# Kernel tuning notes

Measured on AMD Instinct MI355X. Metric: run time of the kernel, lower is better.

The kernel has to match this reference:

```python
import jax, jax.numpy as jnp
import numpy as np
from jax import lax

B, T, H, L, NV = 2048, 100, 256, 128, 5  # batch, max_len, hidden, latent, len(NUC_VOCAB)


def setup_inputs() -> dict:
    key = jax.random.key(0)
    ks = jax.random.split(key, 13)
    s = 0.05
    inp = {
        "x_seq": jax.random.uniform(ks[0], (B, T, NV), dtype=jnp.float32),
        "hidden_states": jax.random.normal(ks[1], (B, H), dtype=jnp.float32) * 0.1,
        "tree_latent_vec": jax.random.normal(ks[2], (B, L), dtype=jnp.float32),
        "graph_latent_vec": jax.random.normal(ks[3], (B, L), dtype=jnp.float32),
        "lengths": jnp.maximum(1, jax.random.randint(ks[4], (B,), 0, T + 1)).astype(jnp.int32),
        # concat_squash_linear: (H + L) -> H
        "W_cs": jax.random.normal(ks[5], (H + L, H), dtype=jnp.float32) * s,
        "b_cs": jnp.zeros((H,), dtype=jnp.float32),
        # GRU cell linears: (H + NV) -> H, acting on cat([x, h])
        "W_z": jax.random.normal(ks[6], (NV + H, H), dtype=jnp.float32) * s,
        "b_z": jnp.zeros((H,), dtype=jnp.float32),
        "W_r": jax.random.normal(ks[7], (NV + H, H), dtype=jnp.float32) * s,
        "b_r": jnp.zeros((H,), dtype=jnp.float32),
        "W_h": jax.random.normal(ks[8], (NV + H, H), dtype=jnp.float32) * s,
        "b_h": jnp.zeros((H,), dtype=jnp.float32),
    }
    return inp


def _decode(x_seq, hidden_states, tree_latent_vec, graph_latent_vec, lengths,
            W_cs, b_cs, W_z, b_z, W_r, b_r, W_h, b_h):
    # concat volatile hidden state with graph latent, squash back to H
    h0 = jax.nn.relu(jnp.concatenate([hidden_states, graph_latent_vec], axis=-1) @ W_cs + b_cs)

    def gru_step(h, x):  # h: [B,H], x: [B,NV]
        xh = jnp.concatenate([x, h], axis=-1)          # [B, NV+H]
        z = jax.nn.sigmoid(xh @ W_z + b_z)
        r = jax.nn.sigmoid(xh @ W_r + b_r)
        xg = jnp.concatenate([x, r * h], axis=-1)
        pre_h = jnp.tanh(xg @ W_h + b_h)
        new_h = (1.0 - z) * h + z * pre_h
        return new_h, new_h

    _, hs = lax.scan(gru_step, h0, jnp.swapaxes(x_seq, 0, 1))  # [T,B,H]
    all_h = jnp.swapaxes(hs, 0, 1)                              # [B,T,H]

    # gather hidden state at last valid timestep (pre_padding_idx)
    new_h = jnp.take_along_axis(all_h, (lengths - 1)[:, None, None], axis=1)[:, 0]  # [B,H]

    # per-segment max-pool over valid positions (segment_representation)
    mask = jnp.arange(T)[None, :] < lengths[:, None]            # [B,T]
    seg_rep = jnp.max(jnp.where(mask[:, :, None], all_h, -jnp.inf), axis=1)  # [B,H]

    # depadded token features concatenated with per-batch tree/graph latents;
    # kept padded [B,T,.] with zeros at invalid positions (fixed-shape form)
    tok = jnp.concatenate([
        all_h,
        jnp.broadcast_to(tree_latent_vec[:, None, :], (B, T, L)),
        jnp.broadcast_to(graph_latent_vec[:, None, :], (B, T, L)),
    ], axis=-1)                                                 # [B,T,H+2L]
    all_hidden_states = jnp.where(mask[:, :, None], tok, 0.0)
    return new_h, all_hidden_states, seg_rep


def reference(x_seq, hidden_states, tree_latent_vec, graph_latent_vec, lengths,
              W_cs, b_cs, W_z, b_z, W_r, b_r, W_h, b_h):
    return _decode(x_seq, hidden_states, tree_latent_vec, graph_latent_vec, lengths,
                   W_cs, b_cs, W_z, b_z, W_r, b_r, W_h, b_h)
```

## Files before the change

kernel.cpp:

```cpp
#include <hip/hip_runtime.h>
#include <stdint.h>

#define B_N 2048
#define T_N 100
#define H_N 256
#define L_N 128
#define NV_N 5
#define COLS (H_N + 2 * 128)

#define KXH 261
#define KPAD 264
#define KCS 384
#define RB 8
#define NKQ 8
#define KQ_LEN 33
#define CH 11

static constexpr long long OUT_ALLH = (long long)B_N * H_N;
static constexpr long long OUT_SEG  = OUT_ALLH + (long long)B_N * T_N * COLS;

static constexpr int SMEM_FLOATS = 2 * NKQ * RB * H_N + 2 * KPAD * RB;
static constexpr int SMEM_BYTES  = SMEM_FLOATS * 4;

__device__ __forceinline__ float bits2f(uint32_t u) {
    union { uint32_t u; float f; } v; v.u = u; return v.f;
}
__device__ __forceinline__ uint16_t f2bf(float f) {
    union { float f; uint32_t u; } v; v.f = f;
    uint32_t r = (v.u + 0x7FFFu + ((v.u >> 16) & 1u)) >> 16;
    return (uint16_t)r;
}

__device__ __forceinline__ int detect_f32(const uint32_t* __restrict__ w) {
    int cnt = 0;
    #pragma unroll 8
    for (int i = 0; i < 64; ++i) {
        uint32_t e = (w[i] >> 23) & 0xFFu;
        cnt += (e >= 97u && e <= 130u) ? 1 : 0;
    }
    return cnt >= 32 ? 1 : 0;
}

template <bool F32> struct IO;

template <> struct IO<true> {
    using Raw = float4;
    static __device__ __forceinline__ Raw ldraw(const void* p, long long idx) {
        return *(const float4*)((const float*)p + idx);
    }
    static __device__ __forceinline__ void cvt(const Raw& u, float f[4]) {
        f[0] = u.x; f[1] = u.y; f[2] = u.z; f[3] = u.w;
    }
    static __device__ __forceinline__ void ld4(const void* p, long long idx, float f[4]) {
        const float4 v = *(const float4*)((const float*)p + idx);
        f[0] = v.x; f[1] = v.y; f[2] = v.z; f[3] = v.w;
    }
    static __device__ __forceinline__ float ld1(const void* p, long long idx) {
        return ((const float*)p)[idx];
    }
    static __device__ __forceinline__ void st4(void* p, long long idx, const float f[4]) {
        *(float4*)((float*)p + idx) = make_float4(f[0], f[1], f[2], f[3]);
    }
    static __device__ __forceinline__ void st4z(void* p, long long idx) {
        *(float4*)((float*)p + idx) = make_float4(0.f, 0.f, 0.f, 0.f);
    }
};

template <> struct IO<false> {
    using Raw = uint2;
    static __device__ __forceinline__ Raw ldraw(const void* p, long long idx) {
        return *(const uint2*)((const uint16_t*)p + idx);
    }
    static __device__ __forceinline__ void cvt(const Raw& u, float f[4]) {
        f[0] = bits2f(u.x << 16);
        f[1] = bits2f(u.x & 0xFFFF0000u);
        f[2] = bits2f(u.y << 16);
        f[3] = bits2f(u.y & 0xFFFF0000u);
    }
    static __device__ __forceinline__ void ld4(const void* p, long long idx, float f[4]) {
        uint2 u = *(const uint2*)((const uint16_t*)p + idx);
        cvt(u, f);
    }
    static __device__ __forceinline__ float ld1(const void* p, long long idx) {
        return bits2f(((uint32_t)((const uint16_t*)p)[idx]) << 16);
    }
    static __device__ __forceinline__ void st4(void* p, long long idx, const float f[4]) {
        uint2 u;
        u.x = (uint32_t)f2bf(f[0]) | ((uint32_t)f2bf(f[1]) << 16);
        u.y = (uint32_t)f2bf(f[2]) | ((uint32_t)f2bf(f[3]) << 16);
        *(uint2*)((uint16_t*)p + idx) = u;
    }
    static __device__ __forceinline__ void st4z(void* p, long long idx) {
        *(uint2*)((uint16_t*)p + idx) = make_uint2(0u, 0u);
    }
};

__device__ __forceinline__ float sigmoid_f(float x) {
    x = fminf(fmaxf(x, -30.f), 30.f);
    return 1.f / (1.f + __expf(-x));
}
__device__ __forceinline__ float tanh_f(float x) {
    x = fminf(fmaxf(x, -15.f), 15.f);
    float e = __expf(-2.f * x);
    return (1.f - e) / (1.f + e);
}

template <bool F32>
__global__ __launch_bounds__(256) void latent_fill_kernel(
    const void* __restrict__ tree,
    const void* __restrict__ graph,
    const int* __restrict__ lengths,
    const void* __restrict__ Wcs_detect,
    void* __restrict__ out)
{
    __shared__ int s_is32;
    if (threadIdx.x == 0) s_is32 = detect_f32((const uint32_t*)Wcs_detect);
    __syncthreads();
    if ((s_is32 != 0) != F32) return;

    long long idx = (long long)blockIdx.x * 256 + threadIdx.x;
    int c = ((int)(idx & 31)) * 8;
    long long bt = idx >> 5;
    int t = (int)(bt % T_N);
    int b = (int)(bt / T_N);

    long long dst = OUT_ALLH + bt * COLS + H_N + c;
    if (t < lengths[b]) {
        float v[8];
        if (c < L_N) {
            IO<F32>::ld4(tree, (long long)b * L_N + c, v);
            IO<F32>::ld4(tree, (long long)b * L_N + c + 4, v + 4);
        } else {
            IO<F32>::ld4(graph, (long long)b * L_N + (c - L_N), v);
            IO<F32>::ld4(graph, (long long)b * L_N + (c - L_N) + 4, v + 4);
        }
        IO<F32>::st4(out, dst, v);
        IO<F32>::st4(out, dst + 4, v + 4);
    } else {
        IO<F32>::st4z(out, dst);
        IO<F32>::st4z(out, dst + 4);
    }
}

template <bool F32>
__global__ __launch_bounds__(512, 2) void gru_kernel(
    const void* __restrict__ x_seq,
    const void* __restrict__ hidden,
    const void* __restrict__ graph,
    const int* __restrict__ lengths,
    const void* __restrict__ Wcs, const void* __restrict__ bcs,
    const void* __restrict__ Wz,  const void* __restrict__ bz,
    const void* __restrict__ Wr,  const void* __restrict__ br,
    const void* __restrict__ Wh,  const void* __restrict__ bh,
    void* __restrict__ out)
{
    extern __shared__ float smem[];
    float* Pz  = smem;
    float* Pr  = Pz  + NKQ * RB * H_N;
    float* xhT = Pr  + NKQ * RB * H_N;
    float* xgT = xhT + KPAD * RB;

    __shared__ int s_is32;
    __shared__ int s_len[RB];
    if (threadIdx.x == 0) s_is32 = detect_f32((const uint32_t*)Wcs);
    __syncthreads();
    if ((s_is32 != 0) != F32) return;

    const int tid  = threadIdx.x;
    const int wv   = tid >> 6;
    const int lane = tid & 63;
    const int c0   = lane * 4;

    if (tid < RB) {
        int L = lengths[blockIdx.x * RB + tid];
        s_len[tid] = min(max(L, 1), T_N);
    }
    if (tid < (KPAD - KXH) * RB) {
        int p = tid / RB, r = tid - p * RB;
        xhT[(KXH + p) * RB + r] = 0.f;
        xgT[(KXH + p) * RB + r] = 0.f;
    }
    __syncthreads();

    const int b0  = blockIdx.x * RB;
    const int bo  = b0 + wv;
    const int len = s_len[wv];
    int maxlen = 1;
    #pragma unroll
    for (int i = 0; i < RB; ++i) maxlen = max(maxlen, s_len[i]);

    {
        float* cs = Pz;
        for (int i = tid; i < RB * KCS; i += 512) {
            int r = i / KCS;
            int k = i - r * KCS;
            int bb = b0 + r;
            float v = (k < H_N) ? IO<F32>::ld1(hidden, (long long)bb * H_N + k)
                                : IO<F32>::ld1(graph,  (long long)bb * L_N + (k - H_N));
            cs[r * 388 + k] = v;
        }
    }
    __syncthreads();

    float h[4];
    {
        const float* cs = Pz;
        float acc[4];
        IO<F32>::ld4(bcs, c0, acc);
        for (int k = 0; k < KCS; k += 4) {
            const float4 hv = *reinterpret_cast<const float4*>(&cs[wv * 388 + k]);
            float hvv[4] = {hv.x, hv.y, hv.z, hv.w};
            #pragma unroll
            for (int kk = 0; kk < 4; ++kk) {
                float w[4];
                IO<F32>::ld4(Wcs, (long long)(k + kk) * H_N + c0, w);
                #pragma unroll
                for (int j = 0; j < 4; ++j) acc[j] += hvv[kk] * w[j];
            }
        }
        #pragma unroll
        for (int j = 0; j < 4; ++j) h[j] = fmaxf(acc[j], 0.f);
    }
    __syncthreads();

    float bzv[4], brv[4], bhv[4];
    IO<F32>::ld4(bz, c0, bzv);
    IO<F32>::ld4(br, c0, brv);
    IO<F32>::ld4(bh, c0, bhv);

    float smax[4] = {-1e30f, -1e30f, -1e30f, -1e30f};

    const int xr = tid / NV_N;
    const int xi = tid - xr * NV_N;
    float xv = 0.f;
    if (tid < RB * NV_N)
        xv = IO<F32>::ld1(x_seq, ((long long)(b0 + xr) * T_N + 0) * NV_N + xi);

    if (tid < RB * NV_N) {
        xhT[xi * RB + xr] = xv;
        xgT[xi * RB + xr] = xv;
    }
    #pragma unroll
    for (int j = 0; j < 4; ++j)
        xhT[(NV_N + c0 + j) * RB + wv] = h[j];
    if (tid < RB * NV_N) {
        int tn = (1 < T_N) ? 1 : 0;
        xv = IO<F32>::ld1(x_seq, ((long long)(b0 + xr) * T_N + tn) * NV_N + xi);
    }
    __syncthreads();

    const int k0 = wv * KQ_LEN;

    float z[4];

    for (int t = 0; t < maxlen; ++t) {
        float az[8][4], ar[8][4];
        #pragma unroll
        for (int r = 0; r < 8; ++r)
            #pragma unroll
            for (int j = 0; j < 4; ++j) { az[r][j] = 0.f; ar[r][j] = 0.f; }

        #pragma unroll 1
        for (int ch = 0; ch < 3; ++ch) {
            const int kb = k0 + ch * CH;
            typename IO<F32>::Raw rz[CH], rr[CH];
            #pragma unroll
            for (int i = 0; i < CH; ++i) {
                const int k  = kb + i;
                const int kl = (k <= KXH - 1) ? k : (KXH - 1);
                rz[i] = IO<F32>::ldraw(Wz, (long long)kl * H_N + c0);
                rr[i] = IO<F32>::ldraw(Wr, (long long)kl * H_N + c0);
            }
            #pragma unroll
            for (int i = 0; i < CH; ++i) {
                const int k = kb + i;
                const float4 a = *reinterpret_cast<const float4*>(&xhT[k * RB + 0]);
                const float4 b = *reinterpret_cast<const float4*>(&xhT[k * RB + 4]);
                float hv[8] = {a.x, a.y, a.z, a.w, b.x, b.y, b.z, b.w};
                float wz4[4], wr4[4];
                IO<F32>::cvt(rz[i], wz4);
                IO<F32>::cvt(rr[i], wr4);
                #pragma unroll
                for (int r = 0; r < 8; ++r) {
                    #pragma unroll
                    for (int j = 0; j < 4; ++j) {
                        az[r][j] += hv[r] * wz4[j];
                        ar[r][j] += hv[r] * wr4[j];
                    }
                }
            }
        }
        #pragma unroll
        for (int r = 0; r < 8; ++r) {
            *reinterpret_cast<float4*>(&Pz[(wv * RB + r) * H_N + c0]) =
                make_float4(az[r][0], az[r][1], az[r][2], az[r][3]);
            *reinterpret_cast<float4*>(&Pr[(wv * RB + r) * H_N + c0]) =
                make_float4(ar[r][0], ar[r][1], ar[r][2], ar[r][3]);
        }
        __syncthreads();

        {
            float sz[4] = {bzv[0], bzv[1], bzv[2], bzv[3]};
            float sr[4] = {brv[0], brv[1], brv[2], brv[3]};
            #pragma unroll
            for (int kq = 0; kq < NKQ; ++kq) {
                const float4 pz = *reinterpret_cast<const float4*>(&Pz[(kq * RB + wv) * H_N + c0]);
                const float4 pr = *reinterpret_cast<const float4*>(&Pr[(kq * RB + wv) * H_N + c0]);
                sz[0] += pz.x; sz[1] += pz.y; sz[2] += pz.z; sz[3] += pz.w;
                sr[0] += pr.x; sr[1] += pr.y; sr[2] += pr.z; sr[3] += pr.w;
            }
            #pragma unroll
            for (int j = 0; j < 4; ++j) {
                z[j] = sigmoid_f(sz[j]);
                float rr = sigmoid_f(sr[j]);
                xgT[(NV_N + c0 + j) * RB + wv] = rr * h[j];
            }
        }
        __syncthreads();

        float ag[8][4];
        #pragma unroll
        for (int r = 0; r < 8; ++r)
            #pragma unroll
            for (int j = 0; j < 4; ++j) ag[r][j] = 0.f;

        #pragma unroll 1
        for (int ch = 0; ch < 3; ++ch) {
            const int kb = k0 + ch * CH;
            typename IO<F32>::Raw rh[CH];
            #pragma unroll
            for (int i = 0; i < CH; ++i) {
                const int k  = kb + i;
                const int kl = (k <= KXH - 1) ? k : (KXH - 1);
                rh[i] = IO<F32>::ldraw(Wh, (long long)kl * H_N + c0);
            }
            #pragma unroll
            for (int i = 0; i < CH; ++i) {
                const int k = kb + i;
                const float4 a = *reinterpret_cast<const float4*>(&xgT[k * RB + 0]);
                const float4 b = *reinterpret_cast<const float4*>(&xgT[k * RB + 4]);
                float gv[8] = {a.x, a.y, a.z, a.w, b.x, b.y, b.z, b.w};
                float wh4[4];
                IO<F32>::cvt(rh[i], wh4);
                #pragma unroll
                for (int r = 0; r < 8; ++r) {
                    #pragma unroll
                    for (int j = 0; j < 4; ++j) ag[r][j] += gv[r] * wh4[j];
                }
            }
        }
        #pragma unroll
        for (int r = 0; r < 8; ++r)
            *reinterpret_cast<float4*>(&Pz[(wv * RB + r) * H_N + c0]) =
                make_float4(ag[r][0], ag[r][1], ag[r][2], ag[r][3]);
        __syncthreads();

        {
            float sg[4] = {bhv[0], bhv[1], bhv[2], bhv[3]};
            #pragma unroll
            for (int kq = 0; kq < NKQ; ++kq) {
                const float4 pg = *reinterpret_cast<const float4*>(&Pz[(kq * RB + wv) * H_N + c0]);
                sg[0] += pg.x; sg[1] += pg.y; sg[2] += pg.z; sg[3] += pg.w;
            }
            const bool active = (t < len);
            float hs[4];
            #pragma unroll
            for (int j = 0; j < 4; ++j) {
                float pre = tanh_f(sg[j]);
                float hn  = (1.f - z[j]) * h[j] + z[j] * pre;
                hn = active ? hn : h[j];
                h[j]  = hn;
                hs[j] = active ? hn : 0.f;
                smax[j] = active ? fmaxf(smax[j], hn) : smax[j];
                xhT[(NV_N + c0 + j) * RB + wv] = hn;
            }
            IO<F32>::st4(out, OUT_ALLH + ((long long)bo * T_N + t) * COLS + c0, hs);
            if (t == len - 1)
                IO<F32>::st4(out, (long long)bo * H_N + c0, h);
        }
        if (tid < RB * NV_N) {
            xhT[xi * RB + xr] = xv;
            xgT[xi * RB + xr] = xv;
            int tn = (t + 2 < T_N) ? (t + 2) : (T_N - 1);
            xv = IO<F32>::ld1(x_seq, ((long long)(b0 + xr) * T_N + tn) * NV_N + xi);
        }
        __syncthreads();
    }

    for (int t = maxlen; t < T_N; ++t)
        IO<F32>::st4z(out, OUT_ALLH + ((long long)bo * T_N + t) * COLS + c0);

    IO<F32>::st4(out, OUT_SEG + (long long)bo * H_N + c0, smax);
}

extern "C" void kernel_launch(void* const* d_in, const int* in_sizes, int n_in,
                              void* d_out, int out_size, void* d_ws, size_t ws_size,
                              hipStream_t stream) {
    const void* x_seq  = d_in[0];
    const void* hidden = d_in[1];
    const void* tree   = d_in[2];
    const void* graph  = d_in[3];
    const int*  lens   = (const int*)d_in[4];
    const void* Wcs    = d_in[5];
    const void* bcs    = d_in[6];
    const void* Wz     = d_in[7];
    const void* bz     = d_in[8];
    const void* Wr     = d_in[9];
    const void* br     = d_in[10];
    const void* Wh     = d_in[11];
    const void* bh     = d_in[12];
    void* out = d_out;

    static bool attr_set = false;
    if (!attr_set) {
        (void)hipFuncSetAttribute(reinterpret_cast<const void*>(&gru_kernel<true>),
                                  hipFuncAttributeMaxDynamicSharedMemorySize, SMEM_BYTES);
        (void)hipFuncSetAttribute(reinterpret_cast<const void*>(&gru_kernel<false>),
                                  hipFuncAttributeMaxDynamicSharedMemorySize, SMEM_BYTES);
        attr_set = true;
    }

    long long work = (long long)B_N * T_N * 32;
    int fill_blocks = (int)(work / 256);

    hipLaunchKernelGGL((latent_fill_kernel<true>),  dim3(fill_blocks), dim3(256), 0, stream,
                       tree, graph, lens, Wcs, out);
    hipLaunchKernelGGL((latent_fill_kernel<false>), dim3(fill_blocks), dim3(256), 0, stream,
                       tree, graph, lens, Wcs, out);

    hipLaunchKernelGGL((gru_kernel<true>), dim3(B_N / RB), dim3(512), SMEM_BYTES, stream,
                       x_seq, hidden, graph, lens,
                       Wcs, bcs, Wz, bz, Wr, br, Wh, bh, out);
    hipLaunchKernelGGL((gru_kernel<false>), dim3(B_N / RB), dim3(512), SMEM_BYTES, stream,
                       x_seq, hidden, graph, lens,
                       Wcs, bcs, Wz, bz, Wr, br, Wh, bh, out);
}
```

Measured before the change: 4.499 ms.

## Double-buffer GRU weight loads in registers across chunks and phases

Replaces the per-chunk load-then-compute loops with a manually software-pipelined schedule. The next chunk's Wz/Wr/Wh weights are loaded into a second register buffer while the current chunk is consumed, and the first chunk of the next phase is prefetched before each barrier. The aim is to hide global/L2 weight-load latency that the serial recurrence otherwise exposes. To hold the extra register buffers, launch bounds drop to one block of 512 per CU, which halves potential occupancy.

```diff
diff --git a/kernel.cpp b/kernel.cpp
--- a/kernel.cpp
+++ b/kernel.cpp
@@ -143,7 +143,7 @@
 }
 
 template <bool F32>
-__global__ __launch_bounds__(512, 2) void gru_kernel(
+__global__ __launch_bounds__(512, 1) void gru_kernel(
     const void* __restrict__ x_seq,
     const void* __restrict__ hidden,
     const void* __restrict__ graph,
@@ -253,6 +253,66 @@
 
     float z[4];
 
+    typename IO<F32>::Raw rzA[CH], rrA[CH], rzB[CH], rrB[CH];
+    typename IO<F32>::Raw rhA[CH], rhB[CH];
+
+#define P1_ISSUE(CHN, RZ, RR)                                               \
+    { const int kb_ = k0 + (CHN) * CH;                                      \
+      _Pragma("unroll")                                                     \
+      for (int i_ = 0; i_ < CH; ++i_) {                                     \
+          const int k_  = kb_ + i_;                                         \
+          const int kl_ = (k_ <= KXH - 1) ? k_ : (KXH - 1);                 \
+          RZ[i_] = IO<F32>::ldraw(Wz, (long long)kl_ * H_N + c0);           \
+          RR[i_] = IO<F32>::ldraw(Wr, (long long)kl_ * H_N + c0);           \
+      } }
+
+#define P1_CONSUME(CHN, RZ, RR)                                             \
+    { const int kb_ = k0 + (CHN) * CH;                                      \
+      _Pragma("unroll")                                                     \
+      for (int i_ = 0; i_ < CH; ++i_) {                                     \
+          const int k_ = kb_ + i_;                                          \
+          const float4 a4_ = *reinterpret_cast<const float4*>(&xhT[k_ * RB + 0]); \
+          const float4 b4_ = *reinterpret_cast<const float4*>(&xhT[k_ * RB + 4]); \
+          float hv_[8] = {a4_.x, a4_.y, a4_.z, a4_.w, b4_.x, b4_.y, b4_.z, b4_.w}; \
+          float wz4_[4], wr4_[4];                                           \
+          IO<F32>::cvt(RZ[i_], wz4_);                                       \
+          IO<F32>::cvt(RR[i_], wr4_);                                       \
+          _Pragma("unroll")                                                 \
+          for (int r_ = 0; r_ < 8; ++r_) {                                  \
+              _Pragma("unroll")                                             \
+              for (int j_ = 0; j_ < 4; ++j_) {                              \
+                  az[r_][j_] += hv_[r_] * wz4_[j_];                         \
+                  ar[r_][j_] += hv_[r_] * wr4_[j_];                         \
+              } } } }
+
+#define P2_ISSUE(CHN, RH)                                                   \
+    { const int kb_ = k0 + (CHN) * CH;                                      \
+      _Pragma("unroll")                                                     \
+      for (int i_ = 0; i_ < CH; ++i_) {                                     \
+          const int k_  = kb_ + i_;                                         \
+          const int kl_ = (k_ <= KXH - 1) ? k_ : (KXH - 1);                 \
+          RH[i_] = IO<F32>::ldraw(Wh, (long long)kl_ * H_N + c0);           \
+      } }
+
+#define P2_CONSUME(CHN, RH)                                                 \
+    { const int kb_ = k0 + (CHN) * CH;                                      \
+      _Pragma("unroll")                                                     \
+      for (int i_ = 0; i_ < CH; ++i_) {                                     \
+          const int k_ = kb_ + i_;                                          \
+          const float4 a4_ = *reinterpret_cast<const float4*>(&xgT[k_ * RB + 0]); \
+          const float4 b4_ = *reinterpret_cast<const float4*>(&xgT[k_ * RB + 4]); \
+          float gv_[8] = {a4_.x, a4_.y, a4_.z, a4_.w, b4_.x, b4_.y, b4_.z, b4_.w}; \
+          float wh4_[4];                                                    \
+          IO<F32>::cvt(RH[i_], wh4_);                                       \
+          _Pragma("unroll")                                                 \
+          for (int r_ = 0; r_ < 8; ++r_) {                                  \
+              _Pragma("unroll")                                             \
+              for (int j_ = 0; j_ < 4; ++j_)                                \
+                  ag[r_][j_] += gv_[r_] * wh4_[j_];                         \
+          } } }
+
+    P1_ISSUE(0, rzA, rrA)
+
     for (int t = 0; t < maxlen; ++t) {
         float az[8][4], ar[8][4];
         #pragma unroll
@@ -260,36 +320,12 @@
             #pragma unroll
             for (int j = 0; j < 4; ++j) { az[r][j] = 0.f; ar[r][j] = 0.f; }
 
-        #pragma unroll 1
-        for (int ch = 0; ch < 3; ++ch) {
-            const int kb = k0 + ch * CH;
-            typename IO<F32>::Raw rz[CH], rr[CH];
-            #pragma unroll
-            for (int i = 0; i < CH; ++i) {
-                const int k  = kb + i;
-                const int kl = (k <= KXH - 1) ? k : (KXH - 1);
-                rz[i] = IO<F32>::ldraw(Wz, (long long)kl * H_N + c0);
-                rr[i] = IO<F32>::ldraw(Wr, (long long)kl * H_N + c0);
-            }
-            #pragma unroll
-            for (int i = 0; i < CH; ++i) {
-                const int k = kb + i;
-                const float4 a = *reinterpret_cast<const float4*>(&xhT[k * RB + 0]);
-                const float4 b = *reinterpret_cast<const float4*>(&xhT[k * RB + 4]);
-                float hv[8] = {a.x, a.y, a.z, a.w, b.x, b.y, b.z, b.w};
-                float wz4[4], wr4[4];
-                IO<F32>::cvt(rz[i], wz4);
-                IO<F32>::cvt(rr[i], wr4);
-                #pragma unroll
-                for (int r = 0; r < 8; ++r) {
-                    #pragma unroll
-                    for (int j = 0; j < 4; ++j) {
-                        az[r][j] += hv[r] * wz4[j];
-                        ar[r][j] += hv[r] * wr4[j];
-                    }
-                }
-            }
-        }
+        P1_ISSUE(1, rzB, rrB)
+        P1_CONSUME(0, rzA, rrA)
+        P1_ISSUE(2, rzA, rrA)
+        P1_CONSUME(1, rzB, rrB)
+        P1_CONSUME(2, rzA, rrA)
+
         #pragma unroll
         for (int r = 0; r < 8; ++r) {
             *reinterpret_cast<float4*>(&Pz[(wv * RB + r) * H_N + c0]) =
@@ -297,6 +333,7 @@
             *reinterpret_cast<float4*>(&Pr[(wv * RB + r) * H_N + c0]) =
                 make_float4(ar[r][0], ar[r][1], ar[r][2], ar[r][3]);
         }
+        P2_ISSUE(0, rhA)
         __syncthreads();
 
         {
@@ -324,35 +361,17 @@
             #pragma unroll
             for (int j = 0; j < 4; ++j) ag[r][j] = 0.f;
 
-        #pragma unroll 1
-        for (int ch = 0; ch < 3; ++ch) {
-            const int kb = k0 + ch * CH;
-            typename IO<F32>::Raw rh[CH];
-            #pragma unroll
-            for (int i = 0; i < CH; ++i) {
-                const int k  = kb + i;
-                const int kl = (k <= KXH - 1) ? k : (KXH - 1);
-                rh[i] = IO<F32>::ldraw(Wh, (long long)kl * H_N + c0);
-            }
-            #pragma unroll
-            for (int i = 0; i < CH; ++i) {
-                const int k = kb + i;
-                const float4 a = *reinterpret_cast<const float4*>(&xgT[k * RB + 0]);
-                const float4 b = *reinterpret_cast<const float4*>(&xgT[k * RB + 4]);
-                float gv[8] = {a.x, a.y, a.z, a.w, b.x, b.y, b.z, b.w};
-                float wh4[4];
-                IO<F32>::cvt(rh[i], wh4);
-                #pragma unroll
-                for (int r = 0; r < 8; ++r) {
-                    #pragma unroll
-                    for (int j = 0; j < 4; ++j) ag[r][j] += gv[r] * wh4[j];
-                }
-            }
-        }
+        P2_ISSUE(1, rhB)
+        P2_CONSUME(0, rhA)
+        P2_ISSUE(2, rhA)
+        P2_CONSUME(1, rhB)
+        P2_CONSUME(2, rhA)
+
         #pragma unroll
         for (int r = 0; r < 8; ++r)
             *reinterpret_cast<float4*>(&Pz[(wv * RB + r) * H_N + c0]) =
                 make_float4(ag[r][0], ag[r][1], ag[r][2], ag[r][3]);
+        P1_ISSUE(0, rzA, rrA)
         __syncthreads();
 
         {
@@ -386,6 +405,11 @@
         }
         __syncthreads();
     }
+
+#undef P1_ISSUE
+#undef P1_CONSUME
+#undef P2_ISSUE
+#undef P2_CONSUME
 
     for (int t = maxlen; t < T_N; ++t)
         IO<F32>::st4z(out, OUT_ALLH + ((long long)bo * T_N + t) * COLS + c0);
```

New measurement: 5.805 ms. 1.29x slower.
